# Optimization experiments

Hardware: AMD Instinct MI355X
Metric: run time of the kernel (lower is better)

The kernel has to match this reference:

```python
import jax, jax.numpy as jnp
import numpy as np

N_NODES = 20000
BN_EPS = 1e-5


def setup_inputs() -> dict:
    key = jax.random.key(0)
    ks = jax.random.split(key, 8)
    in_dim, half, out_dim, n_edges = 256, 128, 256, 320000
    s = 1.0 / np.sqrt(in_dim)
    return {
        "x": jax.random.normal(ks[0], (N_NODES, in_dim), dtype=jnp.float32),
        "edge_index": jax.random.randint(ks[1], (2, n_edges), 0, N_NODES, dtype=jnp.int64),
        "W_l_f": jax.random.normal(ks[2], (half, in_dim), dtype=jnp.float32) * s,
        "b_l_f": jnp.zeros((half,), dtype=jnp.float32),
        "W_r_f": jax.random.normal(ks[3], (half, in_dim), dtype=jnp.float32) * s,
        "W_l_b": jax.random.normal(ks[4], (half, in_dim), dtype=jnp.float32) * s,
        "b_l_b": jnp.zeros((half,), dtype=jnp.float32),
        "W_r_b": jax.random.normal(ks[5], (half, in_dim), dtype=jnp.float32) * s,
        "gamma": jnp.ones((out_dim,), dtype=jnp.float32),
        "beta": jnp.zeros((out_dim,), dtype=jnp.float32),
    }


def _sage(x, src, dst, W_l, b_l, W_r):
    # mean-aggregate source features at destination nodes (PyG SAGEConv, aggr='mean')
    msg_sum = jax.ops.segment_sum(x[src], dst, num_segments=N_NODES)
    cnt = jax.ops.segment_sum(jnp.ones((src.shape[0],), x.dtype), dst, num_segments=N_NODES)
    aggr = msg_sum / jnp.maximum(cnt, 1.0)[:, None]
    # lin_l(aggr) + lin_r(x); lin_l carries the bias in PyG
    return aggr @ W_l.T + b_l + x @ W_r.T


def reference(x, edge_index, W_l_f, b_l_f, W_r_f, W_l_b, b_l_b, W_r_b, gamma, beta):
    src, dst = edge_index[0], edge_index[1]
    h_fwd = _sage(x, src, dst, W_l_f, b_l_f, W_r_f)
    h_bwd = _sage(x, dst, src, W_l_b, b_l_b, W_r_b)  # flipped edges
    h = jnp.concatenate([h_fwd, h_bwd], axis=-1)  # [N, out_dim]
    # BatchNorm1d in training mode (N > 1), biased variance
    mean = jnp.mean(h, axis=0)
    var = jnp.mean(jnp.square(h - mean), axis=0)
    h = (h - mean) * jax.lax.rsqrt(var + BN_EPS) * gamma + beta
    return jax.nn.relu(h)
```

## Files before the change

### kernel.cpp

```cpp
#include <hip/hip_runtime.h>
#include <hip/hip_bf16.h>

#define N_NODES 20000
#define N_EDGES 320000
#define BN_EPS  1e-5f

#define GEMM_MT  ((N_NODES + 127) / 128)
#define NGEMM    (GEMM_MT * 4)
#define FILLB    625

typedef __attribute__((ext_vector_type(4))) float f32x4;
typedef __attribute__((ext_vector_type(8))) __bf16 bf16x8;
typedef __attribute__((ext_vector_type(4))) unsigned short u16x4;

__device__ __forceinline__ unsigned short f2bf(float f) {
    unsigned int u = __float_as_uint(f);
    u += 0x7fffu + ((u >> 16) & 1u);
    return (unsigned short)(u >> 16);
}
__device__ __forceinline__ float bflo(unsigned int u) { return __uint_as_float(u << 16); }
__device__ __forceinline__ float bfhi(unsigned int u) { return __uint_as_float(u & 0xffff0000u); }

__device__ __forceinline__ void gload_lds16(const void* g, void* l) {
    __builtin_amdgcn_global_load_lds(
        (const __attribute__((address_space(1))) void*)g,
        (__attribute__((address_space(3))) void*)l, 16, 0, 0);
}

__global__ __launch_bounds__(256) void cvt_zero_kernel(
    const float* __restrict__ x,
    const float* __restrict__ Wlf, const float* __restrict__ Wlb,
    const float* __restrict__ Wrf, const float* __restrict__ Wrb,
    unsigned short* __restrict__ Xb, unsigned short* __restrict__ Wb,
    uint4* __restrict__ zp, int zquads)
{
    const int XQ = N_NODES * 256 / 4;
    const int WQ = 128 * 256 / 4;
    const int total = XQ + 4 * WQ + zquads;
    for (int i = blockIdx.x * blockDim.x + threadIdx.x; i < total; i += gridDim.x * blockDim.x) {
        if (i >= XQ + 4 * WQ) {
            zp[i - XQ - 4 * WQ] = make_uint4(0, 0, 0, 0);
            continue;
        }
        const float* sp;
        unsigned short* dp;
        if (i < XQ) {
            sp = x + (size_t)i * 4;
            dp = Xb + (size_t)i * 4;
        } else {
            int w = i - XQ;
            int mat = w / WQ;
            int o = (w - mat * WQ) * 4;
            if      (mat == 0) sp = Wlf + o;
            else if (mat == 1) sp = Wlb + o;
            else if (mat == 2) sp = Wrf + o;
            else               sp = Wrb + o;
            dp = Wb + (size_t)mat * 32768 + o;
        }
        float4 v = *(const float4*)sp;
        u16x4 r = {f2bf(v.x), f2bf(v.y), f2bf(v.z), f2bf(v.w)};
        *(u16x4*)dp = r;
    }
}

__global__ void count_rank_kernel(const int* __restrict__ src, const int* __restrict__ dst,
                                  int* __restrict__ cntF, int* __restrict__ cntB,
                                  unsigned int* __restrict__ rank2) {
    int e = blockIdx.x * blockDim.x + threadIdx.x;
    if (e < N_EDGES) {
        unsigned int p = (unsigned int)atomicAdd(&cntF[dst[e]], 1);
        unsigned int q = (unsigned int)atomicAdd(&cntB[src[e]], 1);
        rank2[e] = p | (q << 16);
    }
}

#define SCAN_PER 20
__global__ __launch_bounds__(1024) void scan_kernel(const int* __restrict__ cntF, int* __restrict__ offF,
                                                    const int* __restrict__ cntB, int* __restrict__ offB) {
    const int* in  = blockIdx.x ? cntB : cntF;
    int*       out = blockIdx.x ? offB : offF;
    int t = threadIdx.x;
    int base = t * SCAN_PER;
    int v[SCAN_PER];
    int sum = 0;
    #pragma unroll
    for (int k = 0; k < SCAN_PER; ++k) {
        int i = base + k;
        int c = (i < N_NODES) ? in[i] : 0;
        v[k] = sum; sum += c;
    }
    __shared__ int sh[1024];
    sh[t] = sum;
    __syncthreads();
    for (int o = 1; o < 1024; o <<= 1) {
        int x = (t >= o) ? sh[t - o] : 0;
        __syncthreads();
        sh[t] += x;
        __syncthreads();
    }
    int pre = t ? sh[t - 1] : 0;
    #pragma unroll
    for (int k = 0; k < SCAN_PER; ++k) {
        int i = base + k;
        if (i < N_NODES) out[i] = pre + v[k];
    }
    if (t == 1023) out[N_NODES] = sh[1023];
}

__global__ __launch_bounds__(256) void gemm_fill_kernel(
    const int* __restrict__ src, const int* __restrict__ dst,
    const int* __restrict__ offF, const int* __restrict__ offB,
    const unsigned int* __restrict__ rank2,
    int* __restrict__ listF, int* __restrict__ listB,
    const unsigned short* __restrict__ Xb, const unsigned short* __restrict__ Wb,
    unsigned short* __restrict__ Y, float* __restrict__ Z)
{
    __shared__ unsigned short As[2][128 * 64];
    __shared__ unsigned short Bs[2][128 * 64];

    if (blockIdx.x >= NGEMM) {
        int t = (blockIdx.x - NGEMM) * 256 + threadIdx.x;
        #pragma unroll
        for (int h = 0; h < 2; ++h) {
            int e = t + h * (N_EDGES / 2);
            int s = src[e], d = dst[e];
            unsigned int r2 = rank2[e];
            listF[offF[d] + (int)(r2 & 0xffffu)] = s;
            listB[offB[s] + (int)(r2 >> 16)] = d;
        }
        return;
    }

    int gb = blockIdx.x;
    int by = gb & 3;
    int mBase = (gb >> 2) * 128;
    int tid = threadIdx.x, lane = tid & 63, wave = tid >> 6;
    int wr = wave >> 1, wc = wave & 1;
    const unsigned short* W = Wb + (size_t)by * 128 * 256;

    f32x4 acc[4][4] = {};

    auto STAGE = [&](int b, int k0) {
        #pragma unroll
        for (int c = 0; c < 4; ++c) {
            int S = c * 256 + tid;
            int row = S >> 3;
            int q = (S & 7) ^ (row & 7);
            int gm = mBase + row; gm = gm < N_NODES ? gm : N_NODES - 1;
            gload_lds16(Xb + (size_t)gm * 256 + k0 + q * 8, &As[b][S * 8]);
            gload_lds16(W + (size_t)row * 256 + k0 + q * 8, &Bs[b][S * 8]);
        }
    };
    auto COMPUTE = [&](int b) {
        #pragma unroll
        for (int ks = 0; ks < 2; ++ks) {
            bf16x8 af[4], bfr[4];
            int sl = ks * 4 + (lane >> 4);
            #pragma unroll
            for (int m = 0; m < 4; ++m) {
                int row = wr * 64 + m * 16 + (lane & 15);
                af[m] = *(const bf16x8*)&As[b][row * 64 + ((sl ^ (row & 7)) * 8)];
            }
            #pragma unroll
            for (int n = 0; n < 4; ++n) {
                int row = wc * 64 + n * 16 + (lane & 15);
                bfr[n] = *(const bf16x8*)&Bs[b][row * 64 + ((sl ^ (row & 7)) * 8)];
            }
            #pragma unroll
            for (int m = 0; m < 4; ++m)
                #pragma unroll
                for (int n = 0; n < 4; ++n)
                    acc[m][n] = __builtin_amdgcn_mfma_f32_16x16x32_bf16(af[m], bfr[n], acc[m][n], 0, 0, 0);
        }
    };

    STAGE(0, 0);
    #pragma unroll
    for (int t = 0; t < 4; ++t) {
        if (t < 3) {
            STAGE((t + 1) & 1, (t + 1) * 64);
            asm volatile("s_waitcnt vmcnt(8)" ::: "memory");
        } else {
            asm volatile("s_waitcnt vmcnt(0)" ::: "memory");
        }
        __builtin_amdgcn_s_barrier();
        __builtin_amdgcn_sched_barrier(0);
        COMPUTE(t & 1);
        __builtin_amdgcn_s_barrier();
    }

    bool toY = by < 2;
    int cBase = (by & 1) * 128 + wc * 64;
    #pragma unroll
    for (int m = 0; m < 4; ++m) {
        int gm0 = mBase + wr * 64 + m * 16 + (lane >> 4) * 4;
        #pragma unroll
        for (int n = 0; n < 4; ++n) {
            int gn = cBase + n * 16 + (lane & 15);
            f32x4 v = acc[m][n];
            #pragma unroll
            for (int j = 0; j < 4; ++j) {
                int gm = gm0 + j;
                if (gm < N_NODES) {
                    if (toY) Y[(size_t)gm * 256 + gn] = f2bf(v[j]);
                    else     Z[(size_t)gm * 256 + gn] = v[j];
                }
            }
        }
    }
}

#define NPW 2
__global__ __launch_bounds__(256) void aggregate_kernel(
    const unsigned short* __restrict__ Y,
    const int* __restrict__ offF, const int* __restrict__ listF,
    const int* __restrict__ offB, const int* __restrict__ listB,
    float* __restrict__ H)
{
    int tid = threadIdx.x, lane = tid & 63, wave = tid >> 6;
    int dir = wave >> 1, half = wave & 1;
    const int* off  = dir ? offB : offF;
    const int* list = dir ? listB : listF;
    int eg = lane >> 4;
    int c16 = lane & 15;
    int nodeBase = blockIdx.x * (2 * NPW) + half * NPW;

    for (int jn = 0; jn < NPW; ++jn) {
        int n = nodeBase + jn;
        int beg = off[n], end = off[n + 1];
        int deg = end - beg;
        float acc[8] = {0.f, 0.f, 0.f, 0.f, 0.f, 0.f, 0.f, 0.f};

        for (int i = beg; i < end; i += 64) {
            int c = end - i; if (c > 64) c = 64;
            int u_l = list[i + (lane < c ? lane : 0)];
            for (int e0 = 0; e0 < c; e0 += 16) {
                uint4 v[4];
                #pragma unroll
                for (int k = 0; k < 4; ++k) {
                    int ei = e0 + k * 4 + eg;
                    int u = __shfl(u_l, ei < c ? ei : 0);
                    v[k] = make_uint4(0u, 0u, 0u, 0u);
                    if (ei < c)
                        v[k] = *(const uint4*)(Y + (size_t)u * 256 + dir * 128 + c16 * 8);
                }
                #pragma unroll
                for (int k = 0; k < 4; ++k) {
                    acc[0] += bflo(v[k].x); acc[1] += bfhi(v[k].x);
                    acc[2] += bflo(v[k].y); acc[3] += bfhi(v[k].y);
                    acc[4] += bflo(v[k].z); acc[5] += bfhi(v[k].z);
                    acc[6] += bflo(v[k].w); acc[7] += bfhi(v[k].w);
                }
            }
        }
        #pragma unroll
        for (int j = 0; j < 8; ++j) {
            acc[j] += __shfl_xor(acc[j], 16);
            acc[j] += __shfl_xor(acc[j], 32);
        }
        float h0 = (eg & 2) ? ((eg & 1) ? acc[6] : acc[4]) : ((eg & 1) ? acc[2] : acc[0]);
        float h1 = (eg & 2) ? ((eg & 1) ? acc[7] : acc[5]) : ((eg & 1) ? acc[3] : acc[1]);
        float inv = 1.f / fmaxf((float)deg, 1.f);
        float2* hp = (float2*)(H + (size_t)n * 256 + dir * 128 + c16 * 8 + eg * 2);
        float2 z = *hp;
        *hp = make_float2(fmaf(h0, inv, z.x), fmaf(h1, inv, z.y));
    }
}

__global__ __launch_bounds__(256) void bn_stats_kernel(const float* __restrict__ H,
                                                       float* __restrict__ stats) {
    int col = threadIdx.x;
    float s1 = 0.f, s2 = 0.f;
    for (int n = blockIdx.x; n < N_NODES; n += gridDim.x) {
        float h = H[(size_t)n * 256 + col];
        s1 += h;
        s2 += h * h;
    }
    atomicAdd(&stats[col], s1);
    atomicAdd(&stats[256 + col], s2);
}

__global__ __launch_bounds__(256) void bn_kernel(
    const float* __restrict__ stats, const float* __restrict__ gamma,
    const float* __restrict__ beta, float* __restrict__ H)
{
    __shared__ float sc[256], sf[256];
    int tid = threadIdx.x;
    {
        float mean = stats[tid] * (1.f / N_NODES);
        float var  = stats[256 + tid] * (1.f / N_NODES) - mean * mean;
        float s = rsqrtf(fmaxf(var, 0.f) + BN_EPS) * gamma[tid];
        sc[tid] = s;
        sf[tid] = beta[tid] - mean * s;
    }
    __syncthreads();
    for (int n = blockIdx.x; n < N_NODES; n += gridDim.x) {
        size_t idx = (size_t)n * 256 + tid;
        float h = H[idx];
        H[idx] = fmaxf(h * sc[tid] + sf[tid], 0.f);
    }
}

extern "C" void kernel_launch(void* const* d_in, const int* in_sizes, int n_in,
                              void* d_out, int out_size, void* d_ws, size_t ws_size,
                              hipStream_t stream) {
    const float* x     = (const float*)d_in[0];
    const int*   edge  = (const int*)d_in[1];
    const float* Wlf   = (const float*)d_in[2];
    const float* Wrf   = (const float*)d_in[4];
    const float* Wlb   = (const float*)d_in[5];
    const float* Wrb   = (const float*)d_in[7];
    const float* gamma = (const float*)d_in[8];
    const float* beta  = (const float*)d_in[9];
    float* out = (float*)d_out;

    const int* src = edge;
    const int* dst = edge + N_EDGES;

    char* ws = (char*)d_ws;
    size_t off = 0;
    auto alloc = [&](size_t bytes) { size_t r = off; off += (bytes + 255) & ~(size_t)255; return r; };
    unsigned short* Y  = (unsigned short*)(ws + alloc((size_t)N_NODES * 256 * 2));
    unsigned short* Xb = (unsigned short*)(ws + alloc((size_t)N_NODES * 256 * 2));
    unsigned short* Wb = (unsigned short*)(ws + alloc((size_t)4 * 128 * 256 * 2));
    int* offF  = (int*)(ws + alloc((size_t)(N_NODES + 1) * 4));
    int* offB  = (int*)(ws + alloc((size_t)(N_NODES + 1) * 4));
    int* listF = (int*)(ws + alloc((size_t)N_EDGES * 4));
    int* listB = (int*)(ws + alloc((size_t)N_EDGES * 4));
    unsigned int* rank2 = (unsigned int*)(ws + alloc((size_t)N_EDGES * 4));
    size_t zbase_off = off;
    int* cntF = (int*)(ws + alloc((size_t)N_NODES * 4));
    int* cntB = (int*)(ws + alloc((size_t)N_NODES * 4));
    float* stats = (float*)(ws + alloc(512 * 4));
    size_t zbytes = off - zbase_off;

    cvt_zero_kernel<<<2048, 256, 0, stream>>>(x, Wlf, Wlb, Wrf, Wrb, Xb, Wb,
                                              (uint4*)(ws + zbase_off), (int)(zbytes / 16));

    count_rank_kernel<<<(N_EDGES + 255) / 256, 256, 0, stream>>>(src, dst, cntF, cntB, rank2);
    scan_kernel<<<2, 1024, 0, stream>>>(cntF, offF, cntB, offB);

    gemm_fill_kernel<<<NGEMM + FILLB, 256, 0, stream>>>(
        src, dst, offF, offB, rank2, listF, listB, Xb, Wb, Y, out);

    aggregate_kernel<<<N_NODES / (2 * NPW), 256, 0, stream>>>(
        Y, offF, listF, offB, listB, out);

    bn_stats_kernel<<<512, 256, 0, stream>>>(out, stats);
    bn_kernel<<<2048, 256, 0, stream>>>(stats, gamma, beta, out);
}
```

Measured before the change: 131.6 us.

## Fuse count+scan into convert kernel, fold BN stats into aggregation, XCD-aware GEMM mapping

```diff
diff --git a/kernel.cpp b/kernel.cpp
--- a/kernel.cpp
+++ b/kernel.cpp
@@ -5,8 +5,10 @@
 #define N_EDGES 320000
 #define BN_EPS  1e-5f
 
+#define CNTB     313
+#define CVTB     512
 #define GEMM_MT  ((N_NODES + 127) / 128)
-#define NGEMM    (GEMM_MT * 4)
+#define NGEMM    640
 #define FILLB    625
 
 typedef __attribute__((ext_vector_type(4))) float f32x4;
@@ -27,21 +29,80 @@
         (__attribute__((address_space(3))) void*)l, 16, 0, 0);
 }
 
-__global__ __launch_bounds__(256) void cvt_zero_kernel(
+__global__ void zero_kernel(uint4* __restrict__ zp, int n) {
+    int i = blockIdx.x * blockDim.x + threadIdx.x;
+    if (i < n) zp[i] = make_uint4(0u, 0u, 0u, 0u);
+}
+
+#define SCAN_PER 20
+__global__ __launch_bounds__(1024) void cvt_count_scan_kernel(
     const float* __restrict__ x,
     const float* __restrict__ Wlf, const float* __restrict__ Wlb,
     const float* __restrict__ Wrf, const float* __restrict__ Wrb,
     unsigned short* __restrict__ Xb, unsigned short* __restrict__ Wb,
-    uint4* __restrict__ zp, int zquads)
+    const int* __restrict__ src, const int* __restrict__ dst,
+    int* __restrict__ cntF, int* __restrict__ cntB,
+    unsigned int* __restrict__ rank2,
+    int* __restrict__ offF, int* __restrict__ offB,
+    int* __restrict__ done)
 {
+    int tid = threadIdx.x;
+
+    if (blockIdx.x < CNTB) {
+        __shared__ int sh[1024];
+        __shared__ int amLast;
+        int e = blockIdx.x * 1024 + tid;
+        if (e < N_EDGES) {
+            unsigned int p = (unsigned int)atomicAdd(&cntF[dst[e]], 1);
+            unsigned int q = (unsigned int)atomicAdd(&cntB[src[e]], 1);
+            rank2[e] = p | (q << 16);
+        }
+        __syncthreads();
+        if (tid == 0) {
+            __threadfence();
+            int old = atomicAdd(done, 1);
+            amLast = (old == CNTB - 1);
+        }
+        __syncthreads();
+        if (!amLast) return;
+        __threadfence();
+
+        for (int pass = 0; pass < 2; ++pass) {
+            const int* in  = pass ? cntB : cntF;
+            int*       out = pass ? offB : offF;
+            int base = tid * SCAN_PER;
+            int v[SCAN_PER];
+            int sum = 0;
+            #pragma unroll
+            for (int k = 0; k < SCAN_PER; ++k) {
+                int i = base + k;
+                int c = (i < N_NODES) ? in[i] : 0;
+                v[k] = sum; sum += c;
+            }
+            sh[tid] = sum;
+            __syncthreads();
+            for (int o = 1; o < 1024; o <<= 1) {
+                int xv = (tid >= o) ? sh[tid - o] : 0;
+                __syncthreads();
+                sh[tid] += xv;
+                __syncthreads();
+            }
+            int pre = tid ? sh[tid - 1] : 0;
+            #pragma unroll
+            for (int k = 0; k < SCAN_PER; ++k) {
+                int i = base + k;
+                if (i < N_NODES) out[i] = pre + v[k];
+            }
+            if (tid == 1023) out[N_NODES] = sh[1023];
+            __syncthreads();
+        }
+        return;
+    }
+
     const int XQ = N_NODES * 256 / 4;
     const int WQ = 128 * 256 / 4;
-    const int total = XQ + 4 * WQ + zquads;
-    for (int i = blockIdx.x * blockDim.x + threadIdx.x; i < total; i += gridDim.x * blockDim.x) {
-        if (i >= XQ + 4 * WQ) {
-            zp[i - XQ - 4 * WQ] = make_uint4(0, 0, 0, 0);
-            continue;
-        }
+    const int total = XQ + 4 * WQ;
+    for (int i = (blockIdx.x - CNTB) * 1024 + tid; i < total; i += CVTB * 1024) {
         const float* sp;
         unsigned short* dp;
         if (i < XQ) {
@@ -63,50 +124,6 @@
     }
 }
 
-__global__ void count_rank_kernel(const int* __restrict__ src, const int* __restrict__ dst,
-                                  int* __restrict__ cntF, int* __restrict__ cntB,
-                                  unsigned int* __restrict__ rank2) {
-    int e = blockIdx.x * blockDim.x + threadIdx.x;
-    if (e < N_EDGES) {
-        unsigned int p = (unsigned int)atomicAdd(&cntF[dst[e]], 1);
-        unsigned int q = (unsigned int)atomicAdd(&cntB[src[e]], 1);
-        rank2[e] = p | (q << 16);
-    }
-}
-
-#define SCAN_PER 20
-__global__ __launch_bounds__(1024) void scan_kernel(const int* __restrict__ cntF, int* __restrict__ offF,
-                                                    const int* __restrict__ cntB, int* __restrict__ offB) {
-    const int* in  = blockIdx.x ? cntB : cntF;
-    int*       out = blockIdx.x ? offB : offF;
-    int t = threadIdx.x;
-    int base = t * SCAN_PER;
-    int v[SCAN_PER];
-    int sum = 0;
-    #pragma unroll
-    for (int k = 0; k < SCAN_PER; ++k) {
-        int i = base + k;
-        int c = (i < N_NODES) ? in[i] : 0;
-        v[k] = sum; sum += c;
-    }
-    __shared__ int sh[1024];
-    sh[t] = sum;
-    __syncthreads();
-    for (int o = 1; o < 1024; o <<= 1) {
-        int x = (t >= o) ? sh[t - o] : 0;
-        __syncthreads();
-        sh[t] += x;
-        __syncthreads();
-    }
-    int pre = t ? sh[t - 1] : 0;
-    #pragma unroll
-    for (int k = 0; k < SCAN_PER; ++k) {
-        int i = base + k;
-        if (i < N_NODES) out[i] = pre + v[k];
-    }
-    if (t == 1023) out[N_NODES] = sh[1023];
-}
-
 __global__ __launch_bounds__(256) void gemm_fill_kernel(
     const int* __restrict__ src, const int* __restrict__ dst,
     const int* __restrict__ offF, const int* __restrict__ offB,
@@ -132,8 +149,11 @@
     }
 
     int gb = blockIdx.x;
-    int by = gb & 3;
-    int mBase = (gb >> 2) * 128;
+    int xcd = gb & 7;
+    int by = (gb >> 3) & 3;
+    int mTile = (gb >> 5) + 20 * xcd;
+    if (mTile >= GEMM_MT) return;
+    int mBase = mTile * 128;
     int tid = threadIdx.x, lane = tid & 63, wave = tid >> 6;
     int wr = wave >> 1, wc = wave & 1;
     const unsigned short* W = Wb + (size_t)by * 128 * 256;
@@ -210,12 +230,12 @@
     }
 }
 
-#define NPW 2
-__global__ __launch_bounds__(256) void aggregate_kernel(
+#define NPW 4
+__global__ __launch_bounds__(256) void aggregate_stats_kernel(
     const unsigned short* __restrict__ Y,
     const int* __restrict__ offF, const int* __restrict__ listF,
     const int* __restrict__ offB, const int* __restrict__ listB,
-    float* __restrict__ H)
+    float* __restrict__ H, float* __restrict__ stats)
 {
     int tid = threadIdx.x, lane = tid & 63, wave = tid >> 6;
     int dir = wave >> 1, half = wave & 1;
@@ -225,15 +245,25 @@
     int c16 = lane & 15;
     int nodeBase = blockIdx.x * (2 * NPW) + half * NPW;
 
+    int begs[NPW], degs[NPW], ul0[NPW];
+    #pragma unroll
     for (int jn = 0; jn < NPW; ++jn) {
         int n = nodeBase + jn;
-        int beg = off[n], end = off[n + 1];
-        int deg = end - beg;
+        int b = off[n], e = off[n + 1];
+        begs[jn] = b; degs[jn] = e - b;
+        int c = e - b; if (c > 64) c = 64;
+        ul0[jn] = list[b + (lane < c ? lane : 0)];
+    }
+
+    float s1a = 0.f, s1b = 0.f, s2a = 0.f, s2b = 0.f;
+
+    #pragma unroll
+    for (int jn = 0; jn < NPW; ++jn) {
+        int n = nodeBase + jn;
+        int deg = degs[jn];
         float acc[8] = {0.f, 0.f, 0.f, 0.f, 0.f, 0.f, 0.f, 0.f};
 
-        for (int i = beg; i < end; i += 64) {
-            int c = end - i; if (c > 64) c = 64;
-            int u_l = list[i + (lane < c ? lane : 0)];
+        auto process = [&](int u_l, int c) {
             for (int e0 = 0; e0 < c; e0 += 16) {
                 uint4 v[4];
                 #pragma unroll
@@ -252,7 +282,15 @@
                     acc[6] += bflo(v[k].w); acc[7] += bfhi(v[k].w);
                 }
             }
-        }
+        };
+
+        process(ul0[jn], deg < 64 ? deg : 64);
+        for (int i = begs[jn] + 64; i < begs[jn] + deg; i += 64) {
+            int c = begs[jn] + deg - i; if (c > 64) c = 64;
+            int u_l = list[i + (lane < c ? lane : 0)];
+            process(u_l, c);
+        }
+
         #pragma unroll
         for (int j = 0; j < 8; ++j) {
             acc[j] += __shfl_xor(acc[j], 16);
@@ -263,21 +301,28 @@
         float inv = 1.f / fmaxf((float)deg, 1.f);
         float2* hp = (float2*)(H + (size_t)n * 256 + dir * 128 + c16 * 8 + eg * 2);
         float2 z = *hp;
-        *hp = make_float2(fmaf(h0, inv, z.x), fmaf(h1, inv, z.y));
-    }
-}
-
-__global__ __launch_bounds__(256) void bn_stats_kernel(const float* __restrict__ H,
-                                                       float* __restrict__ stats) {
-    int col = threadIdx.x;
-    float s1 = 0.f, s2 = 0.f;
-    for (int n = blockIdx.x; n < N_NODES; n += gridDim.x) {
-        float h = H[(size_t)n * 256 + col];
-        s1 += h;
-        s2 += h * h;
-    }
-    atomicAdd(&stats[col], s1);
-    atomicAdd(&stats[256 + col], s2);
+        float v0 = fmaf(h0, inv, z.x);
+        float v1 = fmaf(h1, inv, z.y);
+        *hp = make_float2(v0, v1);
+        s1a += v0; s2a += v0 * v0;
+        s1b += v1; s2b += v1 * v1;
+    }
+
+    __shared__ float red[2][64][4];
+    if (half) {
+        red[dir][lane][0] = s1a; red[dir][lane][1] = s1b;
+        red[dir][lane][2] = s2a; red[dir][lane][3] = s2b;
+    }
+    __syncthreads();
+    if (!half) {
+        s1a += red[dir][lane][0]; s1b += red[dir][lane][1];
+        s2a += red[dir][lane][2]; s2b += red[dir][lane][3];
+        int col = dir * 128 + c16 * 8 + eg * 2;
+        atomicAdd(&stats[col], s1a);
+        atomicAdd(&stats[col + 1], s1b);
+        atomicAdd(&stats[256 + col], s2a);
+        atomicAdd(&stats[256 + col + 1], s2b);
+    }
 }
 
 __global__ __launch_bounds__(256) void bn_kernel(
@@ -331,21 +376,21 @@
     size_t zbase_off = off;
     int* cntF = (int*)(ws + alloc((size_t)N_NODES * 4));
     int* cntB = (int*)(ws + alloc((size_t)N_NODES * 4));
+    int* done = (int*)(ws + alloc(256));
     float* stats = (float*)(ws + alloc(512 * 4));
     size_t zbytes = off - zbase_off;
-
-    cvt_zero_kernel<<<2048, 256, 0, stream>>>(x, Wlf, Wlb, Wrf, Wrb, Xb, Wb,
-                                              (uint4*)(ws + zbase_off), (int)(zbytes / 16));
-
-    count_rank_kernel<<<(N_EDGES + 255) / 256, 256, 0, stream>>>(src, dst, cntF, cntB, rank2);
-    scan_kernel<<<2, 1024, 0, stream>>>(cntF, offF, cntB, offB);
+    int zquads = (int)(zbytes / 16);
+
+    zero_kernel<<<(zquads + 255) / 256, 256, 0, stream>>>((uint4*)(ws + zbase_off), zquads);
+
+    cvt_count_scan_kernel<<<CNTB + CVTB, 1024, 0, stream>>>(
+        x, Wlf, Wlb, Wrf, Wrb, Xb, Wb, src, dst, cntF, cntB, rank2, offF, offB, done);
 
     gemm_fill_kernel<<<NGEMM + FILLB, 256, 0, stream>>>(
         src, dst, offF, offB, rank2, listF, listB, Xb, Wb, Y, out);
 
-    aggregate_kernel<<<N_NODES / (2 * NPW), 256, 0, stream>>>(
-        Y, offF, listF, offB, listB, out);
-
-    bn_stats_kernel<<<512, 256, 0, stream>>>(out, stats);
+    aggregate_stats_kernel<<<N_NODES / (2 * NPW), 256, 0, stream>>>(
+        Y, offF, listF, offB, listB, out, stats);
+
     bn_kernel<<<2048, 256, 0, stream>>>(stats, gamma, beta, out);
 }
```

Result: slower. 245.3 us (+86.4%).
